# Optimization experiments

Measured on AMD Instinct MI355X. Metric: run time of the kernel, lower is better.

## Reference

```python
import jax, jax.numpy as jnp
import numpy as np

ALPHA = 0.25
GAMMA = 2.0
EPS = 1e-8
COST_CLASS = 1.0
COST_BBOX = 1.0
COST_GIOU = 1.0


def segment_cw_to_t1t2(x):
    # x: [..., 2] = (center, width) -> (t1, t2)
    c, w = x[..., 0], x[..., 1]
    return jnp.stack([c - 0.5 * w, c + 0.5 * w], axis=-1)


def segment_iou(a, b):
    # a: [N, 2], b: [M, 2] -> pairwise IoU [N, M]
    lt = jnp.maximum(a[:, None, 0], b[None, :, 0])
    rb = jnp.minimum(a[:, None, 1], b[None, :, 1])
    inter = jnp.clip(rb - lt, 0.0)
    union = (a[:, 1] - a[:, 0])[:, None] + (b[:, 1] - b[:, 0])[None, :] - inter
    return inter / jnp.maximum(union, EPS)


def setup_inputs() -> dict:
    key = jax.random.key(0)
    k1, k2, k3, k4, k5, k6 = jax.random.split(key, 6)
    bs, Q, n_cls, M = 16, 2000, 80, 1024
    pred_logits = jax.random.normal(k1, (bs, Q, n_cls), dtype=jnp.float32)
    # boxes layout: [t1, t2, center, width] with t1<=t2 and width>0 (valid segments)
    p_t = jnp.sort(jax.random.uniform(k2, (bs, Q, 2), dtype=jnp.float32), axis=-1)
    p_cw = jax.random.uniform(k3, (bs, Q, 2), dtype=jnp.float32) * jnp.array([1.0, 0.5]) + jnp.array([0.0, 0.05])
    pred_boxes = jnp.concatenate([p_t, p_cw], axis=-1)
    t_t = jnp.sort(jax.random.uniform(k4, (M, 2), dtype=jnp.float32), axis=-1)
    t_cw = jax.random.uniform(k5, (M, 2), dtype=jnp.float32) * jnp.array([1.0, 0.5]) + jnp.array([0.0, 0.05])
    tgt_bbox = jnp.concatenate([t_t, t_cw], axis=-1)
    tgt_ids = jax.random.randint(k6, (M,), 0, n_cls, dtype=jnp.int64 if jax.config.jax_enable_x64 else jnp.int32)
    return {"pred_logits": pred_logits, "pred_boxes": pred_boxes,
            "tgt_ids": tgt_ids, "tgt_bbox": tgt_bbox}


def reference(pred_logits, pred_boxes, tgt_ids, tgt_bbox):
    bs, Q, _ = pred_logits.shape
    out_prob = jax.nn.softmax(pred_logits.reshape(bs * Q, -1), axis=-1)  # [bs*Q, n_cls]
    out_bbox = pred_boxes.reshape(bs * Q, 4)
    # focal-style classification cost
    neg_cost = (1.0 - ALPHA) * out_prob ** GAMMA * (-jnp.log1p(-out_prob + EPS))
    pos_cost = ALPHA * (1.0 - out_prob) ** GAMMA * (-jnp.log(out_prob + EPS))
    cost_class = pos_cost[:, tgt_ids] - neg_cost[:, tgt_ids]  # [bs*Q, M]
    # L1 box cost (cdist p=1)
    cost_bbox = jnp.sum(jnp.abs(out_bbox[:, None, :] - tgt_bbox[None, :, :]), axis=-1)
    # GIoU-style cost: average of IoU over (c,w)->t1t2 segments and raw t1t2 segments
    cost_giou = -(segment_iou(segment_cw_to_t1t2(out_bbox[:, 2:]), segment_cw_to_t1t2(tgt_bbox[:, 2:]))
                  + segment_iou(out_bbox[:, :2], tgt_bbox[:, :2])) / 2.0
    C = COST_BBOX * cost_bbox + COST_CLASS * cost_class + COST_GIOU * cost_giou
    return C.reshape(bs, Q, -1)
```

## Files before the change

kernel.cpp:

```cpp
#include <hip/hip_runtime.h>
#include <math.h>

#define ALPHA 0.25f
#define EPS 1e-8f

typedef float f4v __attribute__((ext_vector_type(4)));

constexpr int NCLS = 80;
constexpr int Mn = 1024;
constexpr int RPB = 8;
constexpr int NGROUPS = 4000;
constexpr int GRID = 1000;

__global__ __launch_bounds__(256, 5) void matcher_kernel(
    const float* __restrict__ logits,
    const float* __restrict__ pboxes,
    const int*   __restrict__ tids,
    const float* __restrict__ tboxes,
    float* __restrict__ out)
{
    __shared__ float cls[RPB][NCLS];

    const int tid = threadIdx.x;

    const int j0 = tid * 4;
    float t1[4], t2[4], tc[4], th[4], wr[4];
    int id[4];
    #pragma unroll
    for (int k = 0; k < 4; ++k) {
        float4 b = *(const float4*)(tboxes + (size_t)(j0 + k) * 4);
        t1[k] = b.x;
        t2[k] = b.y;
        tc[k] = b.z;
        th[k] = 0.5f * b.w;
        wr[k] = b.y - b.x;
        id[k] = tids[j0 + k];
    }

    for (int G = blockIdx.x; G < NGROUPS; G += GRID) {
        const int row0 = G * RPB;

        if (tid < 160) {
            ((float4*)&cls[0][0])[tid] =
                ((const float4*)(logits + (size_t)row0 * NCLS))[tid];
        }
        __syncthreads();

        {
            const int r = tid >> 5;
            const int c = tid & 31;
            const int c2 = (c < 16) ? c + 64 : c;
            float l0 = cls[r][c];
            float l1 = cls[r][c + 32];
            float l2 = cls[r][c2];
            float e0 = __expf(l0);
            float e1 = __expf(l1);
            float e2 = (c < 16) ? __expf(l2) : 0.0f;
            float s = e0 + e1 + e2;
            #pragma unroll
            for (int off = 16; off; off >>= 1) s += __shfl_xor(s, off);
            float inv_s = __builtin_amdgcn_rcpf(s);
            float p0 = e0 * inv_s, p1 = e1 * inv_s, p2 = e2 * inv_s;
            float o0 = 1.0f - p0, o1 = 1.0f - p1, o2 = 1.0f - p2;
            float cc0 = ALPHA * o0 * o0 * (-__logf(p0 + EPS))
                      - (1.0f - ALPHA) * p0 * p0 * (-__logf(o0 + EPS));
            float cc1 = ALPHA * o1 * o1 * (-__logf(p1 + EPS))
                      - (1.0f - ALPHA) * p1 * p1 * (-__logf(o1 + EPS));
            float cc2 = ALPHA * o2 * o2 * (-__logf(p2 + EPS))
                      - (1.0f - ALPHA) * p2 * p2 * (-__logf(o2 + EPS));
            cls[r][c]      = cc0;
            cls[r][c + 32] = cc1;
            if (c < 16) cls[r][c + 64] = cc2;
        }
        __syncthreads();

        #pragma unroll 2
        for (int r = 0; r < RPB; ++r) {
            const float4 pb = *(const float4*)(pboxes + (size_t)(row0 + r) * 4);
            const float pwr = pb.y - pb.x;
            const float phw = 0.5f * pb.w;

            f4v res;
            #pragma unroll
            for (int k = 0; k < 4; ++k) {
                float d1 = pb.x - t1[k];
                float d2 = pb.y - t2[k];
                float dc = pb.z - tc[k];
                float dw = phw - th[k];
                float ab = fabsf(d1) + fabsf(d2);
                float db = ab + fmaf(fabsf(dw), 2.0f, fabsf(dc));
                float P1 = fmaf(2.0f, th[k], pb.w);
                float A1 = fmaxf(P1 - (fabsf(dc - dw) + fabsf(dc + dw)), 0.0f);
                float D1 = fmaxf(fmaf(2.0f, P1, -A1), 2.0f * EPS);
                float P2 = pwr + wr[k];
                float A2 = fmaxf(P2 - ab, 0.0f);
                float D2 = fmaxf(fmaf(2.0f, P2, -A2), 2.0f * EPS);
                float num = A1 * D2 + A2 * D1;
                float inv = __builtin_amdgcn_rcpf(D1 * D2);
                res[k] = fmaf(num * inv, -0.5f, db + cls[r][id[k]]);
            }
            *(f4v*)(out + (size_t)(row0 + r) * Mn + j0) = res;
        }
        __syncthreads();
    }
}

extern "C" void kernel_launch(void* const* d_in, const int* in_sizes, int n_in,
                              void* d_out, int out_size, void* d_ws, size_t ws_size,
                              hipStream_t stream) {
    const float* logits = (const float*)d_in[0];
    const float* pboxes = (const float*)d_in[1];
    const int*   tids   = (const int*)d_in[2];
    const float* tboxes = (const float*)d_in[3];
    float* out = (float*)d_out;

    matcher_kernel<<<GRID, 256, 0, stream>>>(logits, pboxes, tids, tboxes, out);
}
```

Before: 40.50 us.

## Double-buffer logits in LDS and prefetch next group during box compute

```diff
diff --git a/kernel.cpp b/kernel.cpp
--- a/kernel.cpp
+++ b/kernel.cpp
@@ -8,20 +8,21 @@
 
 constexpr int NCLS = 80;
 constexpr int Mn = 1024;
-constexpr int RPB = 8;
-constexpr int NGROUPS = 4000;
+constexpr int RPG = 8;
+constexpr int GPB = 4;
 constexpr int GRID = 1000;
 
-__global__ __launch_bounds__(256, 5) void matcher_kernel(
+__global__ __launch_bounds__(256, 4) void matcher_kernel(
     const float* __restrict__ logits,
     const float* __restrict__ pboxes,
     const int*   __restrict__ tids,
     const float* __restrict__ tboxes,
     float* __restrict__ out)
 {
-    __shared__ float cls[RPB][NCLS];
+    __shared__ float cls[2][RPG][NCLS];
 
     const int tid = threadIdx.x;
+    const int G0  = blockIdx.x * GPB;
 
     const int j0 = tid * 4;
     float t1[4], t2[4], tc[4], th[4], wr[4];
@@ -37,49 +38,68 @@
         id[k] = tids[j0 + k];
     }
 
-    for (int G = blockIdx.x; G < NGROUPS; G += GRID) {
-        const int row0 = G * RPB;
+    auto softmax_cc = [&](int b) {
+        float* C = &cls[b][0][0];
+        const int r  = tid >> 5;
+        const int c  = tid & 31;
+        const int c2 = (c < 16) ? c + 64 : c;
+        float l0 = C[r * NCLS + c];
+        float l1 = C[r * NCLS + c + 32];
+        float l2 = C[r * NCLS + c2];
+        float e0 = __expf(l0);
+        float e1 = __expf(l1);
+        float e2 = (c < 16) ? __expf(l2) : 0.0f;
+        float s = e0 + e1 + e2;
+        #pragma unroll
+        for (int off = 16; off; off >>= 1) s += __shfl_xor(s, off);
+        float inv_s = __builtin_amdgcn_rcpf(s);
+        float p0 = e0 * inv_s, p1 = e1 * inv_s, p2 = e2 * inv_s;
+        float o0 = 1.0f - p0, o1 = 1.0f - p1, o2 = 1.0f - p2;
+        float cc0 = ALPHA * o0 * o0 * (-__logf(p0 + EPS))
+                  - (1.0f - ALPHA) * p0 * p0 * (-__logf(o0 + EPS));
+        float cc1 = ALPHA * o1 * o1 * (-__logf(p1 + EPS))
+                  - (1.0f - ALPHA) * p1 * p1 * (-__logf(o1 + EPS));
+        float cc2 = ALPHA * o2 * o2 * (-__logf(p2 + EPS))
+                  - (1.0f - ALPHA) * p2 * p2 * (-__logf(o2 + EPS));
+        C[r * NCLS + c]      = cc0;
+        C[r * NCLS + c + 32] = cc1;
+        if (c < 16) C[r * NCLS + c + 64] = cc2;
+    };
 
-        if (tid < 160) {
-            ((float4*)&cls[0][0])[tid] =
-                ((const float4*)(logits + (size_t)row0 * NCLS))[tid];
-        }
-        __syncthreads();
+    if (tid < 160) {
+        f4v v = ((const f4v*)(logits + (size_t)G0 * RPG * NCLS))[tid];
+        ((f4v*)&cls[0][0][0])[tid] = v;
+    }
+    asm volatile("s_waitcnt lgkmcnt(0)" ::: "memory");
+    __builtin_amdgcn_s_barrier();
+    softmax_cc(0);
+    asm volatile("s_waitcnt lgkmcnt(0)" ::: "memory");
+    __builtin_amdgcn_s_barrier();
 
-        {
-            const int r = tid >> 5;
-            const int c = tid & 31;
-            const int c2 = (c < 16) ? c + 64 : c;
-            float l0 = cls[r][c];
-            float l1 = cls[r][c + 32];
-            float l2 = cls[r][c2];
-            float e0 = __expf(l0);
-            float e1 = __expf(l1);
-            float e2 = (c < 16) ? __expf(l2) : 0.0f;
-            float s = e0 + e1 + e2;
+    #pragma unroll 1
+    for (int g = 0; g < GPB; ++g) {
+        const int G    = G0 + g;
+        const int buf  = g & 1;
+        const int row0 = G * RPG;
+        const bool have = (g + 1 < GPB);
+
+        f4v nstg = {0.0f, 0.0f, 0.0f, 0.0f};
+        if (have && tid < 160)
+            nstg = ((const f4v*)(logits + (size_t)(G + 1) * RPG * NCLS))[tid];
+
+        float ccv[RPG][4];
+        #pragma unroll
+        for (int r = 0; r < RPG; ++r)
             #pragma unroll
-            for (int off = 16; off; off >>= 1) s += __shfl_xor(s, off);
-            float inv_s = __builtin_amdgcn_rcpf(s);
-            float p0 = e0 * inv_s, p1 = e1 * inv_s, p2 = e2 * inv_s;
-            float o0 = 1.0f - p0, o1 = 1.0f - p1, o2 = 1.0f - p2;
-            float cc0 = ALPHA * o0 * o0 * (-__logf(p0 + EPS))
-                      - (1.0f - ALPHA) * p0 * p0 * (-__logf(o0 + EPS));
-            float cc1 = ALPHA * o1 * o1 * (-__logf(p1 + EPS))
-                      - (1.0f - ALPHA) * p1 * p1 * (-__logf(o1 + EPS));
-            float cc2 = ALPHA * o2 * o2 * (-__logf(p2 + EPS))
-                      - (1.0f - ALPHA) * p2 * p2 * (-__logf(o2 + EPS));
-            cls[r][c]      = cc0;
-            cls[r][c + 32] = cc1;
-            if (c < 16) cls[r][c + 64] = cc2;
-        }
-        __syncthreads();
+            for (int k = 0; k < 4; ++k)
+                ccv[r][k] = cls[buf][r][id[k]];
 
-        #pragma unroll 2
-        for (int r = 0; r < RPB; ++r) {
+        float* outp = out + (size_t)row0 * Mn + j0;
+        #pragma unroll
+        for (int r = 0; r < RPG; ++r) {
             const float4 pb = *(const float4*)(pboxes + (size_t)(row0 + r) * 4);
             const float pwr = pb.y - pb.x;
             const float phw = 0.5f * pb.w;
-
             f4v res;
             #pragma unroll
             for (int k = 0; k < 4; ++k) {
@@ -90,18 +110,28 @@
                 float ab = fabsf(d1) + fabsf(d2);
                 float db = ab + fmaf(fabsf(dw), 2.0f, fabsf(dc));
                 float P1 = fmaf(2.0f, th[k], pb.w);
-                float A1 = fmaxf(P1 - (fabsf(dc - dw) + fabsf(dc + dw)), 0.0f);
+                float m1 = fmaxf(fabsf(dc), fabsf(dw));
+                float A1 = fmaxf(fmaf(-2.0f, m1, P1), 0.0f);
                 float D1 = fmaxf(fmaf(2.0f, P1, -A1), 2.0f * EPS);
                 float P2 = pwr + wr[k];
                 float A2 = fmaxf(P2 - ab, 0.0f);
                 float D2 = fmaxf(fmaf(2.0f, P2, -A2), 2.0f * EPS);
                 float num = A1 * D2 + A2 * D1;
                 float inv = __builtin_amdgcn_rcpf(D1 * D2);
-                res[k] = fmaf(num * inv, -0.5f, db + cls[r][id[k]]);
+                res[k] = fmaf(num * inv, -0.5f, db + ccv[r][k]);
             }
-            *(f4v*)(out + (size_t)(row0 + r) * Mn + j0) = res;
+            *(f4v*)(outp + (size_t)r * Mn) = res;
         }
-        __syncthreads();
+
+        if (have) {
+            if (tid < 160)
+                ((f4v*)&cls[buf ^ 1][0][0])[tid] = nstg;
+            asm volatile("s_waitcnt lgkmcnt(0)" ::: "memory");
+            __builtin_amdgcn_s_barrier();
+            softmax_cc(buf ^ 1);
+            asm volatile("s_waitcnt lgkmcnt(0)" ::: "memory");
+            __builtin_amdgcn_s_barrier();
+        }
     }
 }
 
```

Result: faster. 38.13 us (-5.8%).
